# Kernel optimization log

Hardware: AMD Instinct MI355X
Metric: run time of the kernel (lower is better)

Reference implementation:

```python
import jax, jax.numpy as jnp
import numpy as np

A, B, I, H, O = 400, 64, 50, 192, 3   # num_agents, batch, input_dim, hidden_dim, output_dim
ADIM, NH = 128, 8                      # attention_dim, num_heads
HD = ADIM // NH
SCALE = HD ** -0.5
EPS = 1e-5


def _ln(x, g, b):
    mu = jnp.mean(x, -1, keepdims=True)
    v = jnp.mean((x - mu) ** 2, -1, keepdims=True)
    return (x - mu) * jax.lax.rsqrt(v + EPS) * g + b


def setup_inputs() -> dict:
    key = jax.random.key(0)
    ks = jax.random.split(key, 12)
    s = 0.05
    n = lambda k, shape: (jax.random.normal(k, shape, jnp.float32) * s)
    return {
        'x': jax.random.normal(ks[0], (B, I), jnp.float32),
        'ln_in_g': jnp.ones((A, I), jnp.float32), 'ln_in_b': jnp.zeros((A, I), jnp.float32),
        'W1': n(ks[1], (A, I, H)), 'b1': jnp.zeros((A, H), jnp.float32),
        'Ws1': n(ks[2], (A, I, H)), 'bs1': jnp.zeros((A, H), jnp.float32),
        'W2': n(ks[3], (A, H, H)), 'b2': jnp.zeros((A, H), jnp.float32),
        'Ws2': n(ks[4], (A, H, H)), 'bs2': jnp.zeros((A, H), jnp.float32),
        'W3': n(ks[5], (A, H, H)), 'b3': jnp.zeros((A, H), jnp.float32),
        'ln_h_g': jnp.ones((A, H), jnp.float32), 'ln_h_b': jnp.zeros((A, H), jnp.float32),
        'Wout': n(ks[6], (A, H, O)), 'bout': jnp.zeros((A, O), jnp.float32),
        'aln_g': jnp.ones((H,), jnp.float32), 'aln_b': jnp.zeros((H,), jnp.float32),
        'Wq': n(ks[7], (H, ADIM)), 'bq': jnp.zeros((ADIM,), jnp.float32),
        'Wk': n(ks[8], (H, ADIM)), 'bk': jnp.zeros((ADIM,), jnp.float32),
        'Wv': n(ks[9], (H, ADIM)), 'bv': jnp.zeros((ADIM,), jnp.float32),
        'Wo': n(ks[10], (ADIM, H)), 'bo': jnp.zeros((H,), jnp.float32),
    }


def _forward(x, ln_in_g, ln_in_b, W1, b1, Ws1, bs1, W2, b2, Ws2, bs2, W3, b3,
             ln_h_g, ln_h_b, Wout, bout, aln_g, aln_b, Wq, bq, Wk, bk, Wv, bv, Wo, bo):
    gelu = lambda t: jax.nn.gelu(t, approximate=False)  # torch F.gelu default = exact erf
    # per-agent input LayerNorm (shared stats, per-agent affine) -> [A, B, I]
    xn = _ln(x[None, :, :], ln_in_g[:, None, :], ln_in_b[:, None, :])
    # agent MLPs as batched GEMMs over agent axis
    h1 = gelu(jnp.einsum('abi,aih->abh', xn, W1) + b1[:, None, :]) \
         + jnp.einsum('abi,aih->abh', xn, Ws1) + bs1[:, None, :]
    h2 = gelu(jnp.einsum('abh,ahk->abk', h1, W2) + b2[:, None, :]) \
         + jnp.einsum('abh,ahk->abk', h1, Ws2) + bs2[:, None, :]
    h3 = _ln(h2 + jnp.einsum('abh,ahk->abk', h2, W3) + b3[:, None, :],
             ln_h_g[:, None, :], ln_h_b[:, None, :])  # [A, B, H]
    # cross-SREK attention across the agent axis
    y = _ln(h3, aln_g, aln_b)
    q = (y @ Wq + bq).reshape(A, B, NH, HD).transpose(1, 2, 0, 3)  # [B, NH, A, HD]
    k = (y @ Wk + bk).reshape(A, B, NH, HD).transpose(1, 2, 0, 3)
    v = (y @ Wv + bv).reshape(A, B, NH, HD).transpose(1, 2, 0, 3)
    attn = jax.nn.softmax(jnp.einsum('bhad,bhcd->bhac', q, k) * SCALE, axis=-1)
    o = jnp.einsum('bhac,bhcd->bhad', attn, v).transpose(2, 0, 1, 3).reshape(A, B, ADIM)
    attended = h3 + (o @ Wo + bo)  # residual (dropout off in eval)
    # per-agent output heads -> [A, B, O]
    logits = jnp.einsum('abh,aho->abo', attended, Wout) + bout[:, None, :]
    return logits


def reference(x, ln_in_g, ln_in_b, W1, b1, Ws1, bs1, W2, b2, Ws2, bs2, W3, b3,
              ln_h_g, ln_h_b, Wout, bout, aln_g, aln_b, Wq, bq, Wk, bk, Wv, bv, Wo, bo):
    return _forward(x, ln_in_g, ln_in_b, W1, b1, Ws1, bs1, W2, b2, Ws2, bs2, W3, b3,
                    ln_h_g, ln_h_b, Wout, bout, aln_g, aln_b, Wq, bq, Wk, bk, Wv, bv, Wo, bo)
```

## Files before the change

kernel.cpp:

```cpp
#include <hip/hip_runtime.h>
#include <math.h>

#define AGENTS 400
#define BATCH  64
#define IDIM   50
#define HDIM   192
#define ODIM   3
#define ADIMM  128
#define NHEADS 8
#define HEADD  16
#define LN_EPS 1e-5f

#define PA   200
#define PAM  192
#define POUT 136

typedef __bf16 bf16x8 __attribute__((ext_vector_type(8)));
typedef float  f32x4  __attribute__((ext_vector_type(4)));

__device__ __forceinline__ float gelu_exact(float x) {
    return 0.5f * x * (1.0f + erff(x * 0.70710678118654752f));
}

__device__ __forceinline__ unsigned pack_bf16x2(float a, float b) {
    unsigned short ua = __builtin_bit_cast(unsigned short, (__bf16)a);
    unsigned short ub = __builtin_bit_cast(unsigned short, (__bf16)b);
    return (unsigned)ua | ((unsigned)ub << 16);
}

__device__ __forceinline__ int as_swz(int row, int col) {
    return ((((col >> 3) ^ (row & 7)) << 3) | (col & 7));
}
__device__ __forceinline__ void st_as(__bf16* As_, int row, int col, float v) {
    As_[row * PAM + as_swz(row, col)] = (__bf16)v;
}
__device__ __forceinline__ float ld_as(const __bf16* As_, int row, int col) {
    return (float)As_[row * PAM + as_swz(row, col)];
}
__device__ __forceinline__ bf16x8 ld_afrag(const __bf16* As_, int row, int k0) {
    int blk = (((k0 >> 3) ^ (row & 7)) << 3);
    return *(const bf16x8*)&As_[row * PAM + blk];
}

#define VMWAIT0()   do { asm volatile("s_waitcnt vmcnt(0)" ::: "memory"); \
                         __builtin_amdgcn_sched_barrier(0); } while (0)
#define BARRIER()   do { __builtin_amdgcn_s_barrier(); \
                         __builtin_amdgcn_sched_barrier(0); } while (0)

struct WPtrs { const float *W1, *Ws1, *W2, *Ws2, *W3; };

__device__ __forceinline__ void issue_slot(int s, float* buf0, float* buf1,
                                           const WPtrs& P, const int* kloc,
                                           const int* nsw, int tid)
{
    const float* M; int c, kdm1;
    if (s < 4)       { M = (s & 1) ? P.Ws1 : P.W1; c = s >> 1;      kdm1 = IDIM - 1; }
    else if (s < 16) { int u = s - 4; M = (u & 1) ? P.Ws2 : P.W2; c = u >> 1; kdm1 = HDIM - 1; }
    else             { M = P.W3; c = s - 16; kdm1 = HDIM - 1; }
    float* dst = (s & 1) ? buf1 : buf0;
    #pragma unroll
    for (int i = 0; i < 6; i++) {
        int kg = c * 32 + kloc[i];
        kg = (kg <= kdm1) ? kg : kdm1;
        const float* src = M + (size_t)kg * HDIM + nsw[i];
        __builtin_amdgcn_global_load_lds(
            (const __attribute__((address_space(1))) void*)src,
            (__attribute__((address_space(3))) void*)(dst + (i * 256 + tid) * 4),
            16, 0, 0);
    }
    __builtin_amdgcn_sched_barrier(0);
}

__device__ __forceinline__ void slot_mfma_f32(f32x4 (&acc)[4][3], const __bf16* As_,
                                              const float* Wbuf, int c, int n0, int lane)
{
    const int r = lane & 15, g = lane >> 4;
    bf16x8 bf[3];
    #pragma unroll
    for (int t = 0; t < 3; t++) {
        int cs = (n0 + 16 * t + r) ^ (g << 3);
        #pragma unroll
        for (int j = 0; j < 8; j++)
            bf[t][j] = (__bf16)Wbuf[(g * 8 + j) * HDIM + cs];
    }
    #pragma unroll
    for (int rg = 0; rg < 4; rg++) {
        bf16x8 af = ld_afrag(As_, 16 * rg + r, c * 32 + g * 8);
        #pragma unroll
        for (int t = 0; t < 3; t++)
            acc[rg][t] = __builtin_amdgcn_mfma_f32_16x16x32_bf16(af, bf[t], acc[rg][t], 0, 0, 0);
    }
}

__global__ __launch_bounds__(256, 2) void mlp_kernel(
    const float* __restrict__ x,
    const float* __restrict__ ln_in_g, const float* __restrict__ ln_in_b,
    const float* __restrict__ W1, const float* __restrict__ b1,
    const float* __restrict__ Ws1, const float* __restrict__ bs1,
    const float* __restrict__ W2, const float* __restrict__ b2,
    const float* __restrict__ Ws2, const float* __restrict__ bs2,
    const float* __restrict__ W3, const float* __restrict__ b3,
    const float* __restrict__ ln_h_g, const float* __restrict__ ln_h_b,
    const float* __restrict__ aln_g, const float* __restrict__ aln_b,
    const float* __restrict__ Wq, const float* __restrict__ bq,
    const float* __restrict__ Wk, const float* __restrict__ bk,
    const float* __restrict__ Wv, const float* __restrict__ bv,
    float* __restrict__ h3out,
    float* __restrict__ qT, float* __restrict__ kT, float* __restrict__ vT)
{
    const int a    = blockIdx.x;
    const int tid  = threadIdx.x;
    const int wave = tid >> 6, lane = tid & 63;
    const int r = lane & 15, g = lane >> 4;
    const int n0 = 48 * wave;

    __shared__ __align__(16) __bf16 As[64 * PAM];
    __shared__ __align__(16) float  Wbuf[2][32 * HDIM];
    __shared__ float mu_s[64], rs_s[64];

    int kloc[6], nsw[6];
    #pragma unroll
    for (int i = 0; i < 6; i++) {
        int w = i * 1024 + tid * 4;
        kloc[i] = w / HDIM;
        int np = w - kloc[i] * HDIM;
        nsw[i] = np ^ (((kloc[i] >> 3) & 3) << 3);
    }

    const WPtrs P = {
        W1  + (size_t)a * IDIM * HDIM,
        Ws1 + (size_t)a * IDIM * HDIM,
        W2  + (size_t)a * HDIM * HDIM,
        Ws2 + (size_t)a * HDIM * HDIM,
        W3  + (size_t)a * HDIM * HDIM };

    {
        int rr = tid >> 2, l = tid & 3;
        float s = 0.f, ss = 0.f;
        for (int k = l; k < IDIM; k += 4) { float v = x[rr * IDIM + k]; s += v; ss += v * v; }
        s  += __shfl_down(s, 2, 4);  s  += __shfl_down(s, 1, 4);
        ss += __shfl_down(ss, 2, 4); ss += __shfl_down(ss, 1, 4);
        if (l == 0) {
            float mu = s * (1.0f / IDIM);
            float var = ss * (1.0f / IDIM) - mu * mu;
            mu_s[rr] = mu;
            rs_s[rr] = rsqrtf(var + LN_EPS);
        }
    }
    __syncthreads();

    issue_slot(0, Wbuf[0], Wbuf[1], P, kloc, nsw, tid);

    for (int sidx = tid; sidx < 64 * 64; sidx += 256) {
        int rr = sidx >> 6, k = sidx & 63;
        float v = 0.f;
        if (k < IDIM)
            v = (x[rr * IDIM + k] - mu_s[rr]) * rs_s[rr] * ln_in_g[a * IDIM + k] + ln_in_b[a * IDIM + k];
        st_as(As, rr, k, v);
    }
    __syncthreads();

    {
        f32x4 acc1[4][3], acc2[4][3];
        #pragma unroll
        for (int i = 0; i < 4; i++)
            #pragma unroll
            for (int t = 0; t < 3; t++) { acc1[i][t] = (f32x4)0.f; acc2[i][t] = (f32x4)0.f; }
        #pragma unroll
        for (int s = 0; s < 4; s++) {
            if (s < 3) issue_slot(s + 1, Wbuf[0], Wbuf[1], P, kloc, nsw, tid);
            if ((s & 1) == 0) slot_mfma_f32(acc1, As, Wbuf[s & 1], s >> 1, n0, lane);
            else              slot_mfma_f32(acc2, As, Wbuf[s & 1], s >> 1, n0, lane);
            VMWAIT0();
            BARRIER();
        }
        issue_slot(4, Wbuf[0], Wbuf[1], P, kloc, nsw, tid);
        #pragma unroll
        for (int t = 0; t < 3; t++) {
            int col = n0 + 16 * t + r;
            float bb  = b1[a * HDIM + col];
            float bbs = bs1[a * HDIM + col];
            #pragma unroll
            for (int rg = 0; rg < 4; rg++)
                #pragma unroll
                for (int i = 0; i < 4; i++) {
                    int row = 16 * rg + 4 * g + i;
                    st_as(As, row, col, gelu_exact(acc1[rg][t][i] + bb) + acc2[rg][t][i] + bbs);
                }
        }
        __syncthreads();
    }

    {
        f32x4 acc1[4][3], acc2[4][3];
        #pragma unroll
        for (int i = 0; i < 4; i++)
            #pragma unroll
            for (int t = 0; t < 3; t++) { acc1[i][t] = (f32x4)0.f; acc2[i][t] = (f32x4)0.f; }
        #pragma unroll
        for (int s = 4; s < 16; s++) {
            if (s < 15) issue_slot(s + 1, Wbuf[0], Wbuf[1], P, kloc, nsw, tid);
            if ((s & 1) == 0) slot_mfma_f32(acc1, As, Wbuf[s & 1], (s - 4) >> 1, n0, lane);
            else              slot_mfma_f32(acc2, As, Wbuf[s & 1], (s - 4) >> 1, n0, lane);
            VMWAIT0();
            BARRIER();
        }
        issue_slot(16, Wbuf[0], Wbuf[1], P, kloc, nsw, tid);
        #pragma unroll
        for (int t = 0; t < 3; t++) {
            int col = n0 + 16 * t + r;
            float bb  = b2[a * HDIM + col];
            float bbs = bs2[a * HDIM + col];
            #pragma unroll
            for (int rg = 0; rg < 4; rg++)
                #pragma unroll
                for (int i = 0; i < 4; i++) {
                    int row = 16 * rg + 4 * g + i;
                    st_as(As, row, col, gelu_exact(acc1[rg][t][i] + bb) + acc2[rg][t][i] + bbs);
                }
        }
        __syncthreads();
    }

    {
        f32x4 acc[4][3];
        #pragma unroll
        for (int i = 0; i < 4; i++)
            #pragma unroll
            for (int t = 0; t < 3; t++) acc[i][t] = (f32x4)0.f;
        #pragma unroll
        for (int s = 16; s < 22; s++) {
            if (s < 21) issue_slot(s + 1, Wbuf[0], Wbuf[1], P, kloc, nsw, tid);
            slot_mfma_f32(acc, As, Wbuf[s & 1], s - 16, n0, lane);
            VMWAIT0();
            BARRIER();
        }
        #pragma unroll
        for (int t = 0; t < 3; t++) {
            int col = n0 + 16 * t + r;
            float bb = b3[a * HDIM + col];
            #pragma unroll
            for (int rg = 0; rg < 4; rg++)
                #pragma unroll
                for (int i = 0; i < 4; i++) {
                    int row = 16 * rg + 4 * g + i;
                    st_as(As, row, col, ld_as(As, row, col) + acc[rg][t][i] + bb);
                }
        }
        __syncthreads();
    }

    {
        int rr = tid >> 2, l = tid & 3;
        float s = 0.f, ss = 0.f;
        for (int k = l; k < HDIM; k += 4) { float v = ld_as(As, rr, k); s += v; ss += v * v; }
        s  += __shfl_down(s, 2, 4);  s  += __shfl_down(s, 1, 4);
        ss += __shfl_down(ss, 2, 4); ss += __shfl_down(ss, 1, 4);
        if (l == 0) {
            float mu = s * (1.0f / HDIM);
            float var = ss * (1.0f / HDIM) - mu * mu;
            mu_s[rr] = mu;
            rs_s[rr] = rsqrtf(var + LN_EPS);
        }
    }
    __syncthreads();
    for (int sidx = tid; sidx < 64 * 48; sidx += 256) {
        int rr = sidx / 48, q = sidx - rr * 48;
        int c = q * 4;
        __bf16* p = &As[rr * PAM + as_swz(rr, c)];
        float4 gv = *(const float4*)&ln_h_g[a * HDIM + c];
        float4 bv = *(const float4*)&ln_h_b[a * HDIM + c];
        float mu = mu_s[rr], rs = rs_s[rr];
        float4 o;
        o.x = ((float)p[0] - mu) * rs * gv.x + bv.x;
        o.y = ((float)p[1] - mu) * rs * gv.y + bv.y;
        o.z = ((float)p[2] - mu) * rs * gv.z + bv.z;
        o.w = ((float)p[3] - mu) * rs * gv.w + bv.w;
        *(float4*)&h3out[((size_t)a * BATCH + rr) * HDIM + c] = o;
        p[0] = (__bf16)o.x; p[1] = (__bf16)o.y; p[2] = (__bf16)o.z; p[3] = (__bf16)o.w;
    }
    __syncthreads();

    {
        int rr = tid >> 2, l = tid & 3;
        float s = 0.f, ss = 0.f;
        for (int k = l; k < HDIM; k += 4) { float v = ld_as(As, rr, k); s += v; ss += v * v; }
        s  += __shfl_down(s, 2, 4);  s  += __shfl_down(s, 1, 4);
        ss += __shfl_down(ss, 2, 4); ss += __shfl_down(ss, 1, 4);
        if (l == 0) {
            float mu = s * (1.0f / HDIM);
            float var = ss * (1.0f / HDIM) - mu * mu;
            mu_s[rr] = mu;
            rs_s[rr] = rsqrtf(var + LN_EPS);
        }
    }
    __syncthreads();
    for (int sidx = tid; sidx < 64 * HDIM; sidx += 256) {
        int rr = sidx / HDIM, c = sidx - rr * HDIM;
        float v = (ld_as(As, rr, c) - mu_s[rr]) * rs_s[rr] * aln_g[c] + aln_b[c];
        st_as(As, rr, c, v);
    }
    __syncthreads();

    #pragma unroll
    for (int p = 0; p < 2; p++) {
        const int nb = 192 * p + 48 * wave;
        const float* wA[3];
        #pragma unroll
        for (int t = 0; t < 3; t++) {
            int nt = nb + 16 * t;
            const float* base = (nt < 128) ? Wq : (nt < 256) ? Wk : Wv;
            wA[t] = base + (nt & 127);
        }
        f32x4 acc[4][3];
        #pragma unroll
        for (int i = 0; i < 4; i++)
            #pragma unroll
            for (int t = 0; t < 3; t++) acc[i][t] = (f32x4)0.f;

        float buf[2][24];
        #pragma unroll
        for (int t = 0; t < 3; t++)
            #pragma unroll
            for (int j = 0; j < 8; j++)
                buf[0][t * 8 + j] = wA[t][(g * 8 + j) * ADIMM + r];
        #pragma unroll
        for (int c = 0; c < 6; c++) {
            const int cur = c & 1, nxt = cur ^ 1;
            if (c < 5) {
                #pragma unroll
                for (int t = 0; t < 3; t++)
                    #pragma unroll
                    for (int j = 0; j < 8; j++)
                        buf[nxt][t * 8 + j] = wA[t][((c + 1) * 32 + g * 8 + j) * ADIMM + r];
            }
            bf16x8 bfr[3];
            #pragma unroll
            for (int t = 0; t < 3; t++)
                #pragma unroll
                for (int j = 0; j < 8; j++)
                    bfr[t][j] = (__bf16)buf[cur][t * 8 + j];
            #pragma unroll
            for (int rg = 0; rg < 4; rg++) {
                bf16x8 af = ld_afrag(As, 16 * rg + r, c * 32 + g * 8);
                #pragma unroll
                for (int t = 0; t < 3; t++)
                    acc[rg][t] = __builtin_amdgcn_mfma_f32_16x16x32_bf16(af, bfr[t], acc[rg][t], 0, 0, 0);
            }
        }

        #pragma unroll
        for (int t = 0; t < 3; t++) {
            int n = nb + 16 * t + r;
            int which = n >> 7, cc = n & 127, hh = cc >> 4, dd = cc & 15;
            const float* bp = (which == 0) ? bq : (which == 1) ? bk : bv;
            float* op = (which == 0) ? qT : (which == 1) ? kT : vT;
            float bb = bp[cc];
            #pragma unroll
            for (int rg = 0; rg < 4; rg++)
                #pragma unroll
                for (int i = 0; i < 4; i++) {
                    int brow = 16 * rg + 4 * g + i;
                    op[(((size_t)brow * NHEADS + hh) * AGENTS + a) * HEADD + dd] = acc[rg][t][i] + bb;
                }
        }
    }
}

template<int NC, int KD, int NT, int NRG, int LDW, int PITCH>
__device__ __forceinline__ void gemm_bpass(f32x4 (&acc)[NRG][NT],
                                           const float* const* wptr,
                                           const __bf16* Asrc, int lane)
{
    const int r = lane & 15, g = lane >> 4;
    float buf[2][NT * 8];

    #pragma unroll
    for (int t = 0; t < NT; t++)
        #pragma unroll
        for (int j = 0; j < 8; j++) {
            int k = g * 8 + j;
            buf[0][t * 8 + j] = (k < KD) ? wptr[t][k * LDW + r] : 0.f;
        }

    #pragma unroll
    for (int c = 0; c < NC; c++) {
        const int cur = c & 1, nxt = cur ^ 1;
        if (c + 1 < NC) {
            #pragma unroll
            for (int t = 0; t < NT; t++)
                #pragma unroll
                for (int j = 0; j < 8; j++) {
                    int k = (c + 1) * 32 + g * 8 + j;
                    buf[nxt][t * 8 + j] = (k < KD) ? wptr[t][k * LDW + r] : 0.f;
                }
        }
        bf16x8 bfr[NT];
        #pragma unroll
        for (int t = 0; t < NT; t++)
            #pragma unroll
            for (int j = 0; j < 8; j++)
                bfr[t][j] = (__bf16)buf[cur][t * 8 + j];
        #pragma unroll
        for (int rg = 0; rg < NRG; rg++) {
            bf16x8 af = *(const bf16x8*)&Asrc[(16 * rg + r) * PITCH + c * 32 + g * 8];
            #pragma unroll
            for (int t = 0; t < NT; t++)
                acc[rg][t] = __builtin_amdgcn_mfma_f32_16x16x32_bf16(af, bfr[t], acc[rg][t], 0, 0, 0);
        }
    }
}

#define PKA 24
#define PVA 408
#define PPA 232

__global__ __launch_bounds__(256, 2) void attn_kernel(
    const float* __restrict__ qT, const float* __restrict__ kT,
    const float* __restrict__ vT, float* __restrict__ oT)
{
    const int bh   = blockIdx.x;
    const int b    = bh >> 3, h = bh & 7;
    const int tid  = threadIdx.x;
    const int wave = tid >> 6, lane = tid & 63;
    const int r = lane & 15, g = lane >> 4;

    __shared__ __align__(16) __bf16 Ks[AGENTS * PKA];
    __shared__ __align__(16) __bf16 Vt[16 * PVA];
    __shared__ __align__(16) __bf16 Ps[4][16 * PPA];

    const float* kp = kT + (size_t)bh * AGENTS * HEADD;
    const float* vp = vT + (size_t)bh * AGENTS * HEADD;
    for (int idx = tid; idx < AGENTS * HEADD; idx += 256) {
        int a_ = idx >> 4, d = idx & 15;
        Ks[a_ * PKA + d] = (__bf16)kp[idx];
        Vt[d * PVA + a_] = (__bf16)vp[idx];
    }
    __bf16* Pw = Ps[wave];
    for (int z = lane; z < 16 * 16; z += 64)
        Pw[(z >> 4) * PPA + 208 + (z & 15)] = (__bf16)0.f;
    __syncthreads();

    for (int mt = wave; mt < 25; mt += 4) {
        const int m0 = mt * 16;

        bf16x8 aq;
        if (g < 2) {
            const float* qp = qT + ((size_t)bh * AGENTS + m0 + r) * HEADD + g * 8;
            #pragma unroll
            for (int j = 0; j < 8; j++) aq[j] = (__bf16)(qp[j] * 0.25f);
        } else {
            #pragma unroll
            for (int j = 0; j < 8; j++) aq[j] = (__bf16)0.f;
        }

        f32x4 sacc[25];
        #pragma unroll
        for (int t = 0; t < 25; t++) {
            bf16x8 bk_ = *(const bf16x8*)&Ks[(t * 16 + r) * PKA + (g & 1) * 8];
            sacc[t] = __builtin_amdgcn_mfma_f32_16x16x32_bf16(aq, bk_, (f32x4)0.f, 0, 0, 0);
        }

        float lv[4];
        #pragma unroll
        for (int i = 0; i < 4; i++) {
            float m_ = sacc[0][i];
            #pragma unroll
            for (int t = 1; t < 25; t++) m_ = fmaxf(m_, sacc[t][i]);
            #pragma unroll
            for (int off = 8; off; off >>= 1) m_ = fmaxf(m_, __shfl_xor(m_, off, 16));
            float l_ = 0.f;
            #pragma unroll
            for (int t = 0; t < 25; t++) {
                float p = __expf(sacc[t][i] - m_);
                sacc[t][i] = p;
                l_ += p;
            }
            #pragma unroll
            for (int off = 8; off; off >>= 1) l_ += __shfl_xor(l_, off, 16);
            lv[i] = l_;
        }

        f32x4 oacc = (f32x4)0.f;

        #pragma unroll
        for (int t = 0; t < 13; t++)
            #pragma unroll
            for (int i = 0; i < 4; i++)
                Pw[(g * 4 + i) * PPA + t * 16 + r] = (__bf16)sacc[t][i];
        __asm__ volatile("s_waitcnt lgkmcnt(0)" ::: "memory");
        #pragma unroll
        for (int c = 0; c < 7; c++) {
            bf16x8 ap  = *(const bf16x8*)&Pw[r * PPA + c * 32 + g * 8];
            bf16x8 bv_ = *(const bf16x8*)&Vt[r * PVA + c * 32 + g * 8];
            oacc = __builtin_amdgcn_mfma_f32_16x16x32_bf16(ap, bv_, oacc, 0, 0, 0);
        }

        for (int z = lane; z < 16 * 16; z += 64)
            Pw[(z >> 4) * PPA + 192 + (z & 15)] = (__bf16)0.f;
        #pragma unroll
        for (int t = 13; t < 25; t++)
            #pragma unroll
            for (int i = 0; i < 4; i++)
                Pw[(g * 4 + i) * PPA + (t - 13) * 16 + r] = (__bf16)sacc[t][i];
        __asm__ volatile("s_waitcnt lgkmcnt(0)" ::: "memory");
        #pragma unroll
        for (int c = 0; c < 6; c++) {
            bf16x8 ap  = *(const bf16x8*)&Pw[r * PPA + c * 32 + g * 8];
            bf16x8 bv_ = *(const bf16x8*)&Vt[r * PVA + 208 + c * 32 + g * 8];
            oacc = __builtin_amdgcn_mfma_f32_16x16x32_bf16(ap, bv_, oacc, 0, 0, 0);
        }

        #pragma unroll
        for (int i = 0; i < 4; i++)
            oT[((size_t)(m0 + g * 4 + i) * BATCH + b) * ADIMM + h * HEADD + r] = oacc[i] / lv[i];
    }
}

__global__ __launch_bounds__(256, 2) void out_kernel(
    const float* __restrict__ h3, const float* __restrict__ oT,
    const float* __restrict__ Wo, const float* __restrict__ bo,
    const float* __restrict__ Wout, const float* __restrict__ bout,
    float* __restrict__ out)
{
    const int a    = blockIdx.x;
    const int tid  = threadIdx.x;
    const int wave = tid >> 6, lane = tid & 63;
    const int r = lane & 15, g = lane >> 4;
    const int n0 = 48 * wave;

    __shared__ __align__(16) __bf16 os[64 * POUT];
    __shared__ __align__(16) __bf16 att[64 * PA];

    for (int idx = tid; idx < 64 * 32; idx += 256) {
        int bb = idx >> 5, q = idx & 31;
        float4 v = ((const float4*)(oT + ((size_t)a * BATCH + bb) * ADIMM))[q];
        unsigned u0 = pack_bf16x2(v.x, v.y);
        unsigned u1 = pack_bf16x2(v.z, v.w);
        *(uint2*)&os[bb * POUT + q * 4] = make_uint2(u0, u1);
    }
    __syncthreads();

    {
        const float* wA[3] = { Wo + n0, Wo + n0 + 16, Wo + n0 + 32 };
        f32x4 acc[4][3];
        #pragma unroll
        for (int i = 0; i < 4; i++)
            #pragma unroll
            for (int t = 0; t < 3; t++) acc[i][t] = (f32x4)0.f;
        gemm_bpass<4, ADIMM, 3, 4, HDIM, POUT>(acc, wA, os, lane);
        #pragma unroll
        for (int t = 0; t < 3; t++) {
            int col = n0 + 16 * t + r;
            float bb = bo[col];
            #pragma unroll
            for (int rg = 0; rg < 4; rg++)
                #pragma unroll
                for (int i = 0; i < 4; i++) {
                    int row = 16 * rg + 4 * g + i;
                    float v = h3[((size_t)a * BATCH + row) * HDIM + col] + acc[rg][t][i] + bb;
                    att[row * PA + col] = (__bf16)v;
                }
        }
    }
    __syncthreads();

    {
        const float* Wp = Wout + (size_t)a * HDIM * ODIM;
        float wb[48];
        #pragma unroll
        for (int c = 0; c < 6; c++)
            #pragma unroll
            for (int j = 0; j < 8; j++) {
                int k = c * 32 + g * 8 + j;
                wb[c * 8 + j] = (r < ODIM) ? Wp[k * ODIM + r] : 0.f;
            }
        f32x4 oacc = (f32x4)0.f;
        #pragma unroll
        for (int c = 0; c < 6; c++) {
            bf16x8 bf;
            #pragma unroll
            for (int j = 0; j < 8; j++) bf[j] = (__bf16)wb[c * 8 + j];
            bf16x8 af = *(const bf16x8*)&att[(16 * wave + r) * PA + c * 32 + g * 8];
            oacc = __builtin_amdgcn_mfma_f32_16x16x32_bf16(af, bf, oacc, 0, 0, 0);
        }
        if (r < ODIM) {
            float bb = bout[a * ODIM + r];
            #pragma unroll
            for (int i = 0; i < 4; i++) {
                int row = 16 * wave + 4 * g + i;
                out[((size_t)a * BATCH + row) * ODIM + r] = oacc[i] + bb;
            }
        }
    }
}

extern "C" void kernel_launch(void* const* d_in, const int* in_sizes, int n_in,
                              void* d_out, int out_size, void* d_ws, size_t ws_size,
                              hipStream_t stream)
{
    const float* x       = (const float*)d_in[0];
    const float* ln_in_g = (const float*)d_in[1];
    const float* ln_in_b = (const float*)d_in[2];
    const float* W1      = (const float*)d_in[3];
    const float* b1      = (const float*)d_in[4];
    const float* Ws1     = (const float*)d_in[5];
    const float* bs1     = (const float*)d_in[6];
    const float* W2      = (const float*)d_in[7];
    const float* b2      = (const float*)d_in[8];
    const float* Ws2     = (const float*)d_in[9];
    const float* bs2     = (const float*)d_in[10];
    const float* W3      = (const float*)d_in[11];
    const float* b3      = (const float*)d_in[12];
    const float* ln_h_g  = (const float*)d_in[13];
    const float* ln_h_b  = (const float*)d_in[14];
    const float* Wout    = (const float*)d_in[15];
    const float* bout    = (const float*)d_in[16];
    const float* aln_g   = (const float*)d_in[17];
    const float* aln_b   = (const float*)d_in[18];
    const float* Wq      = (const float*)d_in[19];
    const float* bq      = (const float*)d_in[20];
    const float* Wk      = (const float*)d_in[21];
    const float* bk      = (const float*)d_in[22];
    const float* Wv      = (const float*)d_in[23];
    const float* bv      = (const float*)d_in[24];
    const float* Wo      = (const float*)d_in[25];
    const float* bo      = (const float*)d_in[26];
    float* out = (float*)d_out;

    float* ws = (float*)d_ws;
    const size_t H3_SZ = (size_t)AGENTS * BATCH * HDIM;
    const size_t QT_SZ = (size_t)BATCH * NHEADS * AGENTS * HEADD;
    float* h3 = ws;
    float* qT = h3 + H3_SZ;
    float* kT = qT + QT_SZ;
    float* vT = kT + QT_SZ;
    float* oT = vT + QT_SZ;

    mlp_kernel<<<AGENTS, 256, 0, stream>>>(x, ln_in_g, ln_in_b,
                                           W1, b1, Ws1, bs1, W2, b2, Ws2, bs2,
                                           W3, b3, ln_h_g, ln_h_b,
                                           aln_g, aln_b, Wq, bq, Wk, bk, Wv, bv,
                                           h3, qT, kT, vT);
    attn_kernel<<<BATCH * NHEADS, 256, 0, stream>>>(qT, kT, vT, oT);
    out_kernel<<<AGENTS, 256, 0, stream>>>(h3, oT, Wo, bo, Wout, bout, out);
}
```

Measured before the change: 361.7 us.

## Vectorize attention loads, prefetch Q, tree-reduce softmax, prefetch h3 and Wout

The attention kernel now loads K/V/Q with float4 reads, prefetches the next tile's Q during the current tile's compute, uses tree reductions for the softmax max and sum, drops a redundant zeroing of the padding, and multiplies by a reciprocal instead of dividing. The output kernel prefetches h3 into registers before the first barrier and stages Wout through shared memory so the global reads are coalesced. The goal is to cut global-memory latency and serial dependency chains, at the cost of more registers (h3v holds 48 floats, plus the qf buffer), which may lower occupancy. Removing the padding zeroing assumes columns 192-207 stay harmless after the first pass.

```diff
diff --git a/kernel.cpp b/kernel.cpp
--- a/kernel.cpp
+++ b/kernel.cpp
@@ -431,28 +431,41 @@
 
     const float* kp = kT + (size_t)bh * AGENTS * HEADD;
     const float* vp = vT + (size_t)bh * AGENTS * HEADD;
-    for (int idx = tid; idx < AGENTS * HEADD; idx += 256) {
-        int a_ = idx >> 4, d = idx & 15;
-        Ks[a_ * PKA + d] = (__bf16)kp[idx];
-        Vt[d * PVA + a_] = (__bf16)vp[idx];
+    for (int idx4 = tid; idx4 < AGENTS * HEADD / 4; idx4 += 256) {
+        int a_ = idx4 >> 2, d0 = (idx4 & 3) << 2;
+        float4 kv = *(const float4*)(kp + a_ * HEADD + d0);
+        float4 vv = *(const float4*)(vp + a_ * HEADD + d0);
+        *(uint2*)&Ks[a_ * PKA + d0] =
+            make_uint2(pack_bf16x2(kv.x, kv.y), pack_bf16x2(kv.z, kv.w));
+        Vt[(d0 + 0) * PVA + a_] = (__bf16)vv.x;
+        Vt[(d0 + 1) * PVA + a_] = (__bf16)vv.y;
+        Vt[(d0 + 2) * PVA + a_] = (__bf16)vv.z;
+        Vt[(d0 + 3) * PVA + a_] = (__bf16)vv.w;
     }
     __bf16* Pw = Ps[wave];
     for (int z = lane; z < 16 * 16; z += 64)
         Pw[(z >> 4) * PPA + 208 + (z & 15)] = (__bf16)0.f;
     __syncthreads();
 
+    float qf[8];
+    auto loadq = [&](int mt_) {
+        if (g < 2) {
+            const float* qp = qT + ((size_t)bh * AGENTS + mt_ * 16 + r) * HEADD + g * 8;
+            float4 v0 = *(const float4*)qp;
+            float4 v1 = *(const float4*)(qp + 4);
+            qf[0] = v0.x; qf[1] = v0.y; qf[2] = v0.z; qf[3] = v0.w;
+            qf[4] = v1.x; qf[5] = v1.y; qf[6] = v1.z; qf[7] = v1.w;
+        }
+    };
+    loadq(wave);
+
     for (int mt = wave; mt < 25; mt += 4) {
         const int m0 = mt * 16;
 
         bf16x8 aq;
-        if (g < 2) {
-            const float* qp = qT + ((size_t)bh * AGENTS + m0 + r) * HEADD + g * 8;
-            #pragma unroll
-            for (int j = 0; j < 8; j++) aq[j] = (__bf16)(qp[j] * 0.25f);
-        } else {
-            #pragma unroll
-            for (int j = 0; j < 8; j++) aq[j] = (__bf16)0.f;
-        }
+        #pragma unroll
+        for (int j = 0; j < 8; j++)
+            aq[j] = (g < 2) ? (__bf16)(qf[j] * 0.25f) : (__bf16)0.f;
 
         f32x4 sacc[25];
         #pragma unroll
@@ -461,21 +474,37 @@
             sacc[t] = __builtin_amdgcn_mfma_f32_16x16x32_bf16(aq, bk_, (f32x4)0.f, 0, 0, 0);
         }
 
+        if (mt + 4 < 25) loadq(mt + 4);
+
         float lv[4];
         #pragma unroll
         for (int i = 0; i < 4; i++) {
-            float m_ = sacc[0][i];
-            #pragma unroll
-            for (int t = 1; t < 25; t++) m_ = fmaxf(m_, sacc[t][i]);
+            float tm[16];
+            #pragma unroll
+            for (int t = 0; t < 9; t++) tm[t] = fmaxf(sacc[t][i], sacc[t + 16][i]);
+            #pragma unroll
+            for (int t = 9; t < 16; t++) tm[t] = sacc[t][i];
+            #pragma unroll
+            for (int off = 8; off; off >>= 1)
+                #pragma unroll
+                for (int t = 0; t < off; t++) tm[t] = fmaxf(tm[t], tm[t + off]);
+            float m_ = tm[0];
             #pragma unroll
             for (int off = 8; off; off >>= 1) m_ = fmaxf(m_, __shfl_xor(m_, off, 16));
-            float l_ = 0.f;
-            #pragma unroll
-            for (int t = 0; t < 25; t++) {
-                float p = __expf(sacc[t][i] - m_);
-                sacc[t][i] = p;
-                l_ += p;
-            }
+
+            #pragma unroll
+            for (int t = 0; t < 25; t++) sacc[t][i] = __expf(sacc[t][i] - m_);
+
+            float ts[16];
+            #pragma unroll
+            for (int t = 0; t < 9; t++) ts[t] = sacc[t][i] + sacc[t + 16][i];
+            #pragma unroll
+            for (int t = 9; t < 16; t++) ts[t] = sacc[t][i];
+            #pragma unroll
+            for (int off = 8; off; off >>= 1)
+                #pragma unroll
+                for (int t = 0; t < off; t++) ts[t] += ts[t + off];
+            float l_ = ts[0];
             #pragma unroll
             for (int off = 8; off; off >>= 1) l_ += __shfl_xor(l_, off, 16);
             lv[i] = l_;
@@ -496,8 +525,6 @@
             oacc = __builtin_amdgcn_mfma_f32_16x16x32_bf16(ap, bv_, oacc, 0, 0, 0);
         }
 
-        for (int z = lane; z < 16 * 16; z += 64)
-            Pw[(z >> 4) * PPA + 192 + (z & 15)] = (__bf16)0.f;
         #pragma unroll
         for (int t = 13; t < 25; t++)
             #pragma unroll
@@ -512,8 +539,10 @@
         }
 
         #pragma unroll
-        for (int i = 0; i < 4; i++)
-            oT[((size_t)(m0 + g * 4 + i) * BATCH + b) * ADIMM + h * HEADD + r] = oacc[i] / lv[i];
+        for (int i = 0; i < 4; i++) {
+            float rl = __builtin_amdgcn_rcpf(lv[i]);
+            oT[((size_t)(m0 + g * 4 + i) * BATCH + b) * ADIMM + h * HEADD + r] = oacc[i] * rl;
+        }
     }
 }
 
@@ -531,6 +560,18 @@
 
     __shared__ __align__(16) __bf16 os[64 * POUT];
     __shared__ __align__(16) __bf16 att[64 * PA];
+    __shared__ __align__(16) float  wout_s[HDIM * ODIM];
+
+    float h3v[3][4][4];
+    #pragma unroll
+    for (int t = 0; t < 3; t++) {
+        int col = n0 + 16 * t + r;
+        #pragma unroll
+        for (int rg = 0; rg < 4; rg++)
+            #pragma unroll
+            for (int i = 0; i < 4; i++)
+                h3v[t][rg][i] = h3[((size_t)a * BATCH + 16 * rg + 4 * g + i) * HDIM + col];
+    }
 
     for (int idx = tid; idx < 64 * 32; idx += 256) {
         int bb = idx >> 5, q = idx & 31;
@@ -539,6 +580,11 @@
         unsigned u1 = pack_bf16x2(v.z, v.w);
         *(uint2*)&os[bb * POUT + q * 4] = make_uint2(u0, u1);
     }
+    {
+        const float4* src = (const float4*)(Wout + (size_t)a * HDIM * ODIM);
+        for (int idx = tid; idx < HDIM * ODIM / 4; idx += 256)
+            ((float4*)wout_s)[idx] = src[idx];
+    }
     __syncthreads();
 
     {
@@ -558,7 +604,7 @@
                 #pragma unroll
                 for (int i = 0; i < 4; i++) {
                     int row = 16 * rg + 4 * g + i;
-                    float v = h3[((size_t)a * BATCH + row) * HDIM + col] + acc[rg][t][i] + bb;
+                    float v = h3v[t][rg][i] + acc[rg][t][i] + bb;
                     att[row * PA + col] = (__bf16)v;
                 }
         }
@@ -566,14 +612,13 @@
     __syncthreads();
 
     {
-        const float* Wp = Wout + (size_t)a * HDIM * ODIM;
         float wb[48];
         #pragma unroll
         for (int c = 0; c < 6; c++)
             #pragma unroll
             for (int j = 0; j < 8; j++) {
                 int k = c * 32 + g * 8 + j;
-                wb[c * 8 + j] = (r < ODIM) ? Wp[k * ODIM + r] : 0.f;
+                wb[c * 8 + j] = (r < ODIM) ? wout_s[k * ODIM + r] : 0.f;
             }
         f32x4 oacc = (f32x4)0.f;
         #pragma unroll
```

Measured after the change: 356.8 us. Within noise of the previous version (-1.3%).
